# Optimization experiments

Hardware: AMD Instinct MI355X
Metric: run time of the kernel (lower is better)

## Reference

```python
import jax, jax.numpy as jnp
import numpy as np

N_NODES = 100000


def _sage_conv(x, edge_index, W_n, W_s, b):
    # edge_index: [2, E] with row0 = src, row1 = dst (messages flow src -> dst)
    src, dst = edge_index[0], edge_index[1]
    msgs = x[src]                                   # [E, F] gather
    summed = jax.ops.segment_sum(msgs, dst, num_segments=N_NODES)   # [N, F]
    deg = jax.ops.segment_sum(jnp.ones((edge_index.shape[1],), x.dtype), dst,
                              num_segments=N_NODES)                 # [N]
    mean = summed / jnp.maximum(deg, 1.0)[:, None]  # mean aggregation
    return mean @ W_n + x @ W_s + b


def setup_inputs() -> dict:
    key = jax.random.key(0)
    ks = jax.random.split(key, 8)
    in_dim, hid_dim, out_dim = 64, 64, 32
    n_edges = 1600000
    x = jax.random.normal(ks[0], (N_NODES, in_dim), dtype=jnp.float32)
    edge_index = jax.random.randint(ks[1], (2, n_edges), 0, N_NODES, dtype=jnp.int64)
    s1 = 1.0 / np.sqrt(in_dim)
    s2 = 1.0 / np.sqrt(hid_dim)
    W1_n = jax.random.uniform(ks[2], (in_dim, hid_dim), jnp.float32, -s1, s1)
    W1_s = jax.random.uniform(ks[3], (in_dim, hid_dim), jnp.float32, -s1, s1)
    b1 = jnp.zeros((hid_dim,), jnp.float32)
    W2_n = jax.random.uniform(ks[4], (hid_dim, out_dim), jnp.float32, -s2, s2)
    W2_s = jax.random.uniform(ks[5], (hid_dim, out_dim), jnp.float32, -s2, s2)
    b2 = jnp.zeros((out_dim,), jnp.float32)
    return {"x": x, "edge_index": edge_index, "W1_n": W1_n, "W1_s": W1_s,
            "b1": b1, "W2_n": W2_n, "W2_s": W2_s, "b2": b2}


def reference(x, edge_index, W1_n, W1_s, b1, W2_n, W2_s, b2):
    h = _sage_conv(x, edge_index, W1_n, W1_s, b1)
    h = jax.nn.relu(h)
    # dropout(p=0.5) is identity in eval mode
    out = _sage_conv(h, edge_index, W2_n, W2_s, b2)
    return out
```

## Files before the change

kernel.cpp:

```cpp
#include <hip/hip_runtime.h>
#include <hip/hip_bf16.h>

#define N_NODES 100000
#define NB 784
#define NPAD 100352
#define BSH 7
#define BMASK 127
#define CAP 4096

typedef float v2f __attribute__((ext_vector_type(2)));

__device__ inline void fma4(float a, const float4& w, float4& c) {
  c.x = fmaf(a, w.x, c.x);
  c.y = fmaf(a, w.y, c.y);
  c.z = fmaf(a, w.z, c.z);
  c.w = fmaf(a, w.w, c.w);
}
__device__ inline unsigned short f2bf(float f) {
  unsigned u = __float_as_uint(f);
  u += 0x7fffu + ((u >> 16) & 1u);
  return (unsigned short)(u >> 16);
}
__device__ inline unsigned pack2bf(float a, float b) {
  return (unsigned)f2bf(a) | ((unsigned)f2bf(b) << 16);
}
__device__ inline float bf2f(unsigned short u) {
  return __uint_as_float((unsigned)u << 16);
}
__device__ inline unsigned packfp8x4(float a, float b, float c, float d) {
  int pk = __builtin_amdgcn_cvt_pk_fp8_f32(a, b, 0, false);
  pk = __builtin_amdgcn_cvt_pk_fp8_f32(c, d, pk, true);
  return (unsigned)pk;
}
__device__ inline float4 relu_mix(uint2 m, uint2 s) {
  float4 v;
  v.x = fmaxf(__uint_as_float(m.x << 16) + __uint_as_float(s.x << 16), 0.f);
  v.y = fmaxf(__uint_as_float(m.x & 0xffff0000u) +
                  __uint_as_float(s.x & 0xffff0000u), 0.f);
  v.z = fmaxf(__uint_as_float(m.y << 16) + __uint_as_float(s.y << 16), 0.f);
  v.w = fmaxf(__uint_as_float(m.y & 0xffff0000u) +
                  __uint_as_float(s.y & 0xffff0000u), 0.f);
  return v;
}

#define EPB 4096
__global__ __launch_bounds__(512) void bscatter_k(const int* __restrict__ src,
                                                  const int* __restrict__ dst,
                                                  unsigned* __restrict__ bcur,
                                                  unsigned* __restrict__ ep,
                                                  int E) {
  __shared__ unsigned lh[NB];
  __shared__ unsigned lbase[NB];
  for (int i = threadIdx.x; i < NB; i += 512) lh[i] = 0;
  __syncthreads();
  const int base = blockIdx.x * EPB;
  unsigned short rank[8];
  unsigned short bb[8];
#pragma unroll
  for (int it = 0; it < 8; ++it) {
    int e = base + it * 512 + threadIdx.x;
    if (e < E) {
      unsigned b = ((unsigned)dst[e]) >> BSH;
      bb[it] = (unsigned short)b;
      rank[it] = (unsigned short)atomicAdd(&lh[b], 1u);
    }
  }
  __syncthreads();
  for (int i = threadIdx.x; i < NB; i += 512)
    lbase[i] = lh[i] ? atomicAdd(&bcur[i], lh[i]) : 0u;
  __syncthreads();
#pragma unroll
  for (int it = 0; it < 8; ++it) {
    int e = base + it * 512 + threadIdx.x;
    if (e < E) {
      unsigned b = bb[it];
      ep[(size_t)b * CAP + lbase[b] + rank[it]] =
          (((unsigned)src[e]) << BSH) | (((unsigned)dst[e]) & BMASK);
    }
  }
}

#define GB1 1563

__global__ __launch_bounds__(256) void fused1_k(
    const float* __restrict__ x, const float* __restrict__ W1n,
    const float* __restrict__ W1s, const float* __restrict__ b1,
    unsigned* __restrict__ xnb8, unsigned short* __restrict__ xsb,
    const unsigned* __restrict__ ep, const unsigned* __restrict__ bcur,
    int* __restrict__ ssrc, uint2* __restrict__ rows2, int M) {
  __shared__ __align__(16) float smem[8192];
  const int tid = threadIdx.x;

  if (blockIdx.x >= GB1) {
    const int b = blockIdx.x - GB1;
    unsigned* cnt = (unsigned*)smem;
    unsigned* sc = cnt + 128;
    const unsigned cntb = bcur[b];
    const unsigned beg = (unsigned)(b * CAP);
    if (tid < 128) cnt[tid] = 0;
    __syncthreads();
    for (unsigned j = tid; j < cntb; j += 256)
      atomicAdd(&cnt[ep[(size_t)beg + j] & BMASK], 1u);
    __syncthreads();
    unsigned v = (tid < 128) ? cnt[tid] : 0u;
    if (tid < 128) sc[tid] = v;
    __syncthreads();
    for (int off = 1; off < 128; off <<= 1) {
      unsigned t = (tid < 128 && tid >= off) ? sc[tid - off] : 0u;
      __syncthreads();
      if (tid < 128) sc[tid] += t;
      __syncthreads();
    }
    if (tid < 128) {
      unsigned ex = sc[tid] - v;
      rows2[b * 128 + tid] = make_uint2(beg + ex, beg + ex + v);
      cnt[tid] = ex;
    }
    __syncthreads();
    for (unsigned j = tid; j < cntb; j += 256) {
      unsigned p = ep[(size_t)beg + j];
      unsigned r = atomicAdd(&cnt[p & BMASK], 1u);
      ssrc[(size_t)beg + r] = (int)(p >> BSH);
    }
    return;
  }

  float* Wn = smem;
  float* Ws = smem + 4096;
  const int row0 = blockIdx.x * 64;

  for (int i = tid; i < 1024; i += 256) {
    ((float4*)Wn)[i] = ((const float4*)W1n)[i];
    ((float4*)Ws)[i] = ((const float4*)W1s)[i];
  }

  const int tx = tid & 15;
  const int ty = tid >> 4;
  const int arow = ty * 4;

  const float* xr[4];
#pragma unroll
  for (int r = 0; r < 4; ++r) {
    long long gr = row0 + arow + r;
    if (gr >= M) gr = M - 1;
    xr[r] = x + gr * 64;
  }

  float4 an[4], as[4];
#pragma unroll
  for (int r = 0; r < 4; ++r) {
    an[r] = make_float4(0.f, 0.f, 0.f, 0.f);
    as[r] = make_float4(0.f, 0.f, 0.f, 0.f);
  }
  __syncthreads();

#pragma unroll 2
  for (int k4 = 0; k4 < 16; ++k4) {
    float4 a[4];
#pragma unroll
    for (int r = 0; r < 4; ++r) a[r] = *(const float4*)(xr[r] + 4 * k4);
    float4 wn0 = *(const float4*)&Wn[(4 * k4 + 0) * 64 + 4 * tx];
    float4 wn1 = *(const float4*)&Wn[(4 * k4 + 1) * 64 + 4 * tx];
    float4 wn2 = *(const float4*)&Wn[(4 * k4 + 2) * 64 + 4 * tx];
    float4 wn3 = *(const float4*)&Wn[(4 * k4 + 3) * 64 + 4 * tx];
    float4 ws0 = *(const float4*)&Ws[(4 * k4 + 0) * 64 + 4 * tx];
    float4 ws1 = *(const float4*)&Ws[(4 * k4 + 1) * 64 + 4 * tx];
    float4 ws2 = *(const float4*)&Ws[(4 * k4 + 2) * 64 + 4 * tx];
    float4 ws3 = *(const float4*)&Ws[(4 * k4 + 3) * 64 + 4 * tx];
#pragma unroll
    for (int r = 0; r < 4; ++r) {
      fma4(a[r].x, wn0, an[r]);
      fma4(a[r].y, wn1, an[r]);
      fma4(a[r].z, wn2, an[r]);
      fma4(a[r].w, wn3, an[r]);
      fma4(a[r].x, ws0, as[r]);
      fma4(a[r].y, ws1, as[r]);
      fma4(a[r].z, ws2, as[r]);
      fma4(a[r].w, ws3, as[r]);
    }
  }

  const float4 bv = *(const float4*)&b1[4 * tx];
#pragma unroll
  for (int r = 0; r < 4; ++r) {
    int row = row0 + arow + r;
    if (row < M) {
      ushort4 ps;
      ps.x = f2bf(as[r].x + bv.x);
      ps.y = f2bf(as[r].y + bv.y);
      ps.z = f2bf(as[r].z + bv.z);
      ps.w = f2bf(as[r].w + bv.w);
      *(ushort4*)&xsb[(long long)row * 64 + 4 * tx] = ps;
      xnb8[(size_t)row * 16 + tx] =
          packfp8x4(an[r].x, an[r].y, an[r].z, an[r].w);
    }
  }
}

__global__ __launch_bounds__(256) void gather1_k(
    const uint4* __restrict__ valb4, const int* __restrict__ ssrc,
    const uint2* __restrict__ rows2, uint4* __restrict__ meanb, int N) {
  constexpr int P = 4;
  const int node = blockIdx.x * 64 + threadIdx.x / P;
  const int p = threadIdx.x & 3;
  if (node >= N) return;
  const uint2 be = rows2[node];
  const unsigned beg = be.x, end = be.y;

  float acc[16];
#pragma unroll
  for (int q = 0; q < 16; ++q) acc[q] = 0.f;

  unsigned j = beg;
  for (; j + 8 <= end; j += 8) {
    int sn[8];
#pragma unroll
    for (int i = 0; i < 8; ++i) sn[i] = ssrc[j + i];
    uint4 u[8];
#pragma unroll
    for (int i = 0; i < 8; ++i) u[i] = valb4[(size_t)sn[i] * P + p];
#pragma unroll
    for (int i = 0; i < 8; ++i) {
      v2f f0 = __builtin_amdgcn_cvt_pk_f32_fp8((int)u[i].x, false);
      v2f f1 = __builtin_amdgcn_cvt_pk_f32_fp8((int)u[i].x, true);
      v2f f2 = __builtin_amdgcn_cvt_pk_f32_fp8((int)u[i].y, false);
      v2f f3 = __builtin_amdgcn_cvt_pk_f32_fp8((int)u[i].y, true);
      v2f f4 = __builtin_amdgcn_cvt_pk_f32_fp8((int)u[i].z, false);
      v2f f5 = __builtin_amdgcn_cvt_pk_f32_fp8((int)u[i].z, true);
      v2f f6 = __builtin_amdgcn_cvt_pk_f32_fp8((int)u[i].w, false);
      v2f f7 = __builtin_amdgcn_cvt_pk_f32_fp8((int)u[i].w, true);
      acc[0] += f0[0];  acc[1] += f0[1];
      acc[2] += f1[0];  acc[3] += f1[1];
      acc[4] += f2[0];  acc[5] += f2[1];
      acc[6] += f3[0];  acc[7] += f3[1];
      acc[8] += f4[0];  acc[9] += f4[1];
      acc[10] += f5[0]; acc[11] += f5[1];
      acc[12] += f6[0]; acc[13] += f6[1];
      acc[14] += f7[0]; acc[15] += f7[1];
    }
  }
  if (j < end) {
    const unsigned last = end - 1;
    int sn[8];
#pragma unroll
    for (int i = 0; i < 8; ++i) {
      unsigned jj = j + i;
      sn[i] = ssrc[jj < last ? jj : last];
    }
    uint4 u[8];
#pragma unroll
    for (int i = 0; i < 8; ++i) u[i] = valb4[(size_t)sn[i] * P + p];
#pragma unroll
    for (int i = 0; i < 8; ++i) {
      float w = ((j + i) < end) ? 1.f : 0.f;
      v2f f0 = __builtin_amdgcn_cvt_pk_f32_fp8((int)u[i].x, false);
      v2f f1 = __builtin_amdgcn_cvt_pk_f32_fp8((int)u[i].x, true);
      v2f f2 = __builtin_amdgcn_cvt_pk_f32_fp8((int)u[i].y, false);
      v2f f3 = __builtin_amdgcn_cvt_pk_f32_fp8((int)u[i].y, true);
      v2f f4 = __builtin_amdgcn_cvt_pk_f32_fp8((int)u[i].z, false);
      v2f f5 = __builtin_amdgcn_cvt_pk_f32_fp8((int)u[i].z, true);
      v2f f6 = __builtin_amdgcn_cvt_pk_f32_fp8((int)u[i].w, false);
      v2f f7 = __builtin_amdgcn_cvt_pk_f32_fp8((int)u[i].w, true);
      acc[0] = fmaf(w, f0[0], acc[0]);   acc[1] = fmaf(w, f0[1], acc[1]);
      acc[2] = fmaf(w, f1[0], acc[2]);   acc[3] = fmaf(w, f1[1], acc[3]);
      acc[4] = fmaf(w, f2[0], acc[4]);   acc[5] = fmaf(w, f2[1], acc[5]);
      acc[6] = fmaf(w, f3[0], acc[6]);   acc[7] = fmaf(w, f3[1], acc[7]);
      acc[8] = fmaf(w, f4[0], acc[8]);   acc[9] = fmaf(w, f4[1], acc[9]);
      acc[10] = fmaf(w, f5[0], acc[10]); acc[11] = fmaf(w, f5[1], acc[11]);
      acc[12] = fmaf(w, f6[0], acc[12]); acc[13] = fmaf(w, f6[1], acc[13]);
      acc[14] = fmaf(w, f7[0], acc[14]); acc[15] = fmaf(w, f7[1], acc[15]);
    }
  }

  const unsigned dg = end - beg;
  const float inv = dg ? 1.f / (float)dg : 0.f;
  uint4 pk0, pk1;
  pk0.x = pack2bf(acc[0] * inv, acc[1] * inv);
  pk0.y = pack2bf(acc[2] * inv, acc[3] * inv);
  pk0.z = pack2bf(acc[4] * inv, acc[5] * inv);
  pk0.w = pack2bf(acc[6] * inv, acc[7] * inv);
  pk1.x = pack2bf(acc[8] * inv, acc[9] * inv);
  pk1.y = pack2bf(acc[10] * inv, acc[11] * inv);
  pk1.z = pack2bf(acc[12] * inv, acc[13] * inv);
  pk1.w = pack2bf(acc[14] * inv, acc[15] * inv);
  meanb[(size_t)node * 8 + 2 * p] = pk0;
  meanb[(size_t)node * 8 + 2 * p + 1] = pk1;
}

__global__ __launch_bounds__(256) void gemm2_k(
    const unsigned short* __restrict__ mean1,
    const unsigned short* __restrict__ xsb, const float* __restrict__ W2n,
    const float* __restrict__ W2s, const float* __restrict__ b2,
    unsigned* __restrict__ hnb8, float* __restrict__ hs, int M) {
  __shared__ float Wn[64 * 32];
  __shared__ float Ws[64 * 32];
  const int tid = threadIdx.x;
  const int row0 = blockIdx.x * 128;

  for (int i = tid; i < 512; i += 256) {
    ((float4*)Wn)[i] = ((const float4*)W2n)[i];
    ((float4*)Ws)[i] = ((const float4*)W2s)[i];
  }

  const int tx = tid & 7;
  const int ty = tid >> 3;
  const int arow = ty * 4;

  const uint2* mp[4];
  const uint2* sp[4];
#pragma unroll
  for (int r = 0; r < 4; ++r) {
    long long gr = row0 + arow + r;
    if (gr >= M) gr = M - 1;
    mp[r] = (const uint2*)(mean1 + gr * 64);
    sp[r] = (const uint2*)(xsb + gr * 64);
  }

  float4 an[4], as[4];
#pragma unroll
  for (int r = 0; r < 4; ++r) {
    an[r] = make_float4(0.f, 0.f, 0.f, 0.f);
    as[r] = make_float4(0.f, 0.f, 0.f, 0.f);
  }
  __syncthreads();

#pragma unroll 2
  for (int k4 = 0; k4 < 16; ++k4) {
    float4 a[4];
#pragma unroll
    for (int r = 0; r < 4; ++r) a[r] = relu_mix(mp[r][k4], sp[r][k4]);
    float4 wn0 = *(const float4*)&Wn[(4 * k4 + 0) * 32 + 4 * tx];
    float4 wn1 = *(const float4*)&Wn[(4 * k4 + 1) * 32 + 4 * tx];
    float4 wn2 = *(const float4*)&Wn[(4 * k4 + 2) * 32 + 4 * tx];
    float4 wn3 = *(const float4*)&Wn[(4 * k4 + 3) * 32 + 4 * tx];
    float4 ws0 = *(const float4*)&Ws[(4 * k4 + 0) * 32 + 4 * tx];
    float4 ws1 = *(const float4*)&Ws[(4 * k4 + 1) * 32 + 4 * tx];
    float4 ws2 = *(const float4*)&Ws[(4 * k4 + 2) * 32 + 4 * tx];
    float4 ws3 = *(const float4*)&Ws[(4 * k4 + 3) * 32 + 4 * tx];
#pragma unroll
    for (int r = 0; r < 4; ++r) {
      fma4(a[r].x, wn0, an[r]);
      fma4(a[r].y, wn1, an[r]);
      fma4(a[r].z, wn2, an[r]);
      fma4(a[r].w, wn3, an[r]);
      fma4(a[r].x, ws0, as[r]);
      fma4(a[r].y, ws1, as[r]);
      fma4(a[r].z, ws2, as[r]);
      fma4(a[r].w, ws3, as[r]);
    }
  }

  const float4 bv = *(const float4*)&b2[4 * tx];
#pragma unroll
  for (int r = 0; r < 4; ++r) {
    int row = row0 + arow + r;
    if (row < M) {
      float4 o;
      o.x = as[r].x + bv.x;
      o.y = as[r].y + bv.y;
      o.z = as[r].z + bv.z;
      o.w = as[r].w + bv.w;
      *(float4*)&hs[(long long)row * 32 + 4 * tx] = o;
      hnb8[(size_t)row * 8 + tx] =
          packfp8x4(an[r].x, an[r].y, an[r].z, an[r].w);
    }
  }
}

__global__ __launch_bounds__(256) void gather2_k(
    const uint4* __restrict__ valb4, const int* __restrict__ ssrc,
    const uint2* __restrict__ rows2, const float* __restrict__ base,
    float* __restrict__ out, int N) {
  constexpr int P = 2;
  const int node = blockIdx.x * 128 + threadIdx.x / P;
  const int p = threadIdx.x & 1;
  if (node >= N) return;
  const uint2 be = rows2[node];
  const unsigned beg = be.x, end = be.y;

  float acc[16];
#pragma unroll
  for (int q = 0; q < 16; ++q) acc[q] = 0.f;

  unsigned j = beg;
  for (; j + 8 <= end; j += 8) {
    int sn[8];
#pragma unroll
    for (int i = 0; i < 8; ++i) sn[i] = ssrc[j + i];
    uint4 u[8];
#pragma unroll
    for (int i = 0; i < 8; ++i) u[i] = valb4[(size_t)sn[i] * P + p];
#pragma unroll
    for (int i = 0; i < 8; ++i) {
      v2f f0 = __builtin_amdgcn_cvt_pk_f32_fp8((int)u[i].x, false);
      v2f f1 = __builtin_amdgcn_cvt_pk_f32_fp8((int)u[i].x, true);
      v2f f2 = __builtin_amdgcn_cvt_pk_f32_fp8((int)u[i].y, false);
      v2f f3 = __builtin_amdgcn_cvt_pk_f32_fp8((int)u[i].y, true);
      v2f f4 = __builtin_amdgcn_cvt_pk_f32_fp8((int)u[i].z, false);
      v2f f5 = __builtin_amdgcn_cvt_pk_f32_fp8((int)u[i].z, true);
      v2f f6 = __builtin_amdgcn_cvt_pk_f32_fp8((int)u[i].w, false);
      v2f f7 = __builtin_amdgcn_cvt_pk_f32_fp8((int)u[i].w, true);
      acc[0] += f0[0];  acc[1] += f0[1];
      acc[2] += f1[0];  acc[3] += f1[1];
      acc[4] += f2[0];  acc[5] += f2[1];
      acc[6] += f3[0];  acc[7] += f3[1];
      acc[8] += f4[0];  acc[9] += f4[1];
      acc[10] += f5[0]; acc[11] += f5[1];
      acc[12] += f6[0]; acc[13] += f6[1];
      acc[14] += f7[0]; acc[15] += f7[1];
    }
  }
  if (j < end) {
    const unsigned last = end - 1;
    int sn[8];
#pragma unroll
    for (int i = 0; i < 8; ++i) {
      unsigned jj = j + i;
      sn[i] = ssrc[jj < last ? jj : last];
    }
    uint4 u[8];
#pragma unroll
    for (int i = 0; i < 8; ++i) u[i] = valb4[(size_t)sn[i] * P + p];
#pragma unroll
    for (int i = 0; i < 8; ++i) {
      float w = ((j + i) < end) ? 1.f : 0.f;
      v2f f0 = __builtin_amdgcn_cvt_pk_f32_fp8((int)u[i].x, false);
      v2f f1 = __builtin_amdgcn_cvt_pk_f32_fp8((int)u[i].x, true);
      v2f f2 = __builtin_amdgcn_cvt_pk_f32_fp8((int)u[i].y, false);
      v2f f3 = __builtin_amdgcn_cvt_pk_f32_fp8((int)u[i].y, true);
      v2f f4 = __builtin_amdgcn_cvt_pk_f32_fp8((int)u[i].z, false);
      v2f f5 = __builtin_amdgcn_cvt_pk_f32_fp8((int)u[i].z, true);
      v2f f6 = __builtin_amdgcn_cvt_pk_f32_fp8((int)u[i].w, false);
      v2f f7 = __builtin_amdgcn_cvt_pk_f32_fp8((int)u[i].w, true);
      acc[0] = fmaf(w, f0[0], acc[0]);   acc[1] = fmaf(w, f0[1], acc[1]);
      acc[2] = fmaf(w, f1[0], acc[2]);   acc[3] = fmaf(w, f1[1], acc[3]);
      acc[4] = fmaf(w, f2[0], acc[4]);   acc[5] = fmaf(w, f2[1], acc[5]);
      acc[6] = fmaf(w, f3[0], acc[6]);   acc[7] = fmaf(w, f3[1], acc[7]);
      acc[8] = fmaf(w, f4[0], acc[8]);   acc[9] = fmaf(w, f4[1], acc[9]);
      acc[10] = fmaf(w, f5[0], acc[10]); acc[11] = fmaf(w, f5[1], acc[11]);
      acc[12] = fmaf(w, f6[0], acc[12]); acc[13] = fmaf(w, f6[1], acc[13]);
      acc[14] = fmaf(w, f7[0], acc[14]); acc[15] = fmaf(w, f7[1], acc[15]);
    }
  }

  const unsigned dg = end - beg;
  const float inv = dg ? 1.f / (float)dg : 0.f;
  const size_t o = (size_t)node * 32 + 16 * p;
#pragma unroll
  for (int q4 = 0; q4 < 4; ++q4) {
    float4 bv = *(const float4*)&base[o + 4 * q4];
    float4 ov;
    ov.x = acc[4 * q4 + 0] * inv + bv.x;
    ov.y = acc[4 * q4 + 1] * inv + bv.y;
    ov.z = acc[4 * q4 + 2] * inv + bv.z;
    ov.w = acc[4 * q4 + 3] * inv + bv.w;
    *(float4*)&out[o + 4 * q4] = ov;
  }
}

extern "C" void kernel_launch(void* const* d_in, const int* in_sizes, int n_in,
                              void* d_out, int out_size, void* d_ws,
                              size_t ws_size, hipStream_t stream) {
  const float* x   = (const float*)d_in[0];
  const int*   ei  = (const int*)d_in[1];
  const float* W1n = (const float*)d_in[2];
  const float* W1s = (const float*)d_in[3];
  const float* b1  = (const float*)d_in[4];
  const float* W2n = (const float*)d_in[5];
  const float* W2s = (const float*)d_in[6];
  const float* b2  = (const float*)d_in[7];
  float* out = (float*)d_out;

  const int E = in_sizes[1] / 2;
  const int M = N_NODES;
  const int* src = ei;
  const int* dst = ei + E;

  char* wsb = (char*)d_ws;
  unsigned*       ep    = (unsigned*)(wsb);
  int*            ssrc  = (int*)(wsb + 12845056);
  uint2*          rows2 = (uint2*)(wsb + 25690112);
  unsigned*       bcur  = (unsigned*)(wsb + 26492928);
  unsigned*       xnb8  = (unsigned*)(wsb + 26496064);
  unsigned short* xsb   = (unsigned short*)(wsb + 32896064);
  unsigned short* mean1 = (unsigned short*)(wsb + 45696064);
  float*          hs    = (float*)(wsb + 58496064);
  unsigned*       hnb8  = (unsigned*)(wsb);

  hipMemsetAsync(bcur, 0, NB * 4, stream);
  bscatter_k<<<(E + EPB - 1) / EPB, 512, 0, stream>>>(src, dst, bcur, ep, E);
  fused1_k<<<GB1 + NB, 256, 0, stream>>>(x, W1n, W1s, b1, xnb8, xsb, ep, bcur,
                                         ssrc, rows2, M);
  gather1_k<<<(M + 63) / 64, 256, 0, stream>>>((const uint4*)xnb8, ssrc, rows2,
                                               (uint4*)mean1, M);
  gemm2_k<<<(M + 127) / 128, 256, 0, stream>>>(mean1, xsb, W2n, W2s, b2, hnb8,
                                               hs, M);
  gather2_k<<<(M + 127) / 128, 256, 0, stream>>>((const uint4*)hnb8, ssrc,
                                                 rows2, hs, out, M);
}
```

Before: 207.8 us.

## Fuse bucket scatter with layer-1 GEMM and gather1 with layer-2 GEMM

Moves the edge bucket-scatter into the same launch as the layer-1 dense transform, and splits the per-bucket sort into its own kernel. It also fuses the first gather with the second layer's GEMM, keeping the mean rows in shared memory instead of writing and re-reading a bf16 mean buffer in global memory. This removes one intermediate buffer round-trip and rebalances launches. The cost is a heavier fused kernel with more shared memory and fewer rows per thread in the GEMM part, which may affect occupancy.

```diff
diff --git a/kernel.cpp b/kernel.cpp
--- a/kernel.cpp
+++ b/kernel.cpp
@@ -44,90 +44,54 @@
 }
 
 #define EPB 4096
-__global__ __launch_bounds__(512) void bscatter_k(const int* __restrict__ src,
-                                                  const int* __restrict__ dst,
-                                                  unsigned* __restrict__ bcur,
-                                                  unsigned* __restrict__ ep,
-                                                  int E) {
-  __shared__ unsigned lh[NB];
-  __shared__ unsigned lbase[NB];
-  for (int i = threadIdx.x; i < NB; i += 512) lh[i] = 0;
-  __syncthreads();
-  const int base = blockIdx.x * EPB;
-  unsigned short rank[8];
-  unsigned short bb[8];
-#pragma unroll
-  for (int it = 0; it < 8; ++it) {
-    int e = base + it * 512 + threadIdx.x;
-    if (e < E) {
-      unsigned b = ((unsigned)dst[e]) >> BSH;
-      bb[it] = (unsigned short)b;
-      rank[it] = (unsigned short)atomicAdd(&lh[b], 1u);
-    }
-  }
-  __syncthreads();
-  for (int i = threadIdx.x; i < NB; i += 512)
-    lbase[i] = lh[i] ? atomicAdd(&bcur[i], lh[i]) : 0u;
-  __syncthreads();
-#pragma unroll
-  for (int it = 0; it < 8; ++it) {
-    int e = base + it * 512 + threadIdx.x;
-    if (e < E) {
-      unsigned b = bb[it];
-      ep[(size_t)b * CAP + lbase[b] + rank[it]] =
-          (((unsigned)src[e]) << BSH) | (((unsigned)dst[e]) & BMASK);
-    }
-  }
-}
-
 #define GB1 1563
 
-__global__ __launch_bounds__(256) void fused1_k(
+__global__ __launch_bounds__(256) void fusedA_k(
+    const int* __restrict__ src, const int* __restrict__ dst,
+    unsigned* __restrict__ bcur, unsigned* __restrict__ ep,
     const float* __restrict__ x, const float* __restrict__ W1n,
     const float* __restrict__ W1s, const float* __restrict__ b1,
     unsigned* __restrict__ xnb8, unsigned short* __restrict__ xsb,
-    const unsigned* __restrict__ ep, const unsigned* __restrict__ bcur,
-    int* __restrict__ ssrc, uint2* __restrict__ rows2, int M) {
+    int E, int NSB, int M) {
   __shared__ __align__(16) float smem[8192];
   const int tid = threadIdx.x;
 
-  if (blockIdx.x >= GB1) {
-    const int b = blockIdx.x - GB1;
-    unsigned* cnt = (unsigned*)smem;
-    unsigned* sc = cnt + 128;
-    const unsigned cntb = bcur[b];
-    const unsigned beg = (unsigned)(b * CAP);
-    if (tid < 128) cnt[tid] = 0;
+  if ((int)blockIdx.x < NSB) {
+    unsigned* lh = (unsigned*)smem;
+    unsigned* lbase = lh + NB;
+    for (int i = tid; i < NB; i += 256) lh[i] = 0;
     __syncthreads();
-    for (unsigned j = tid; j < cntb; j += 256)
-      atomicAdd(&cnt[ep[(size_t)beg + j] & BMASK], 1u);
+    const int base = blockIdx.x * EPB;
+    unsigned short rank[16];
+    unsigned short bb[16];
+#pragma unroll
+    for (int it = 0; it < 16; ++it) {
+      int e = base + it * 256 + tid;
+      if (e < E) {
+        unsigned b = ((unsigned)dst[e]) >> BSH;
+        bb[it] = (unsigned short)b;
+        rank[it] = (unsigned short)atomicAdd(&lh[b], 1u);
+      }
+    }
     __syncthreads();
-    unsigned v = (tid < 128) ? cnt[tid] : 0u;
-    if (tid < 128) sc[tid] = v;
+    for (int i = tid; i < NB; i += 256)
+      lbase[i] = lh[i] ? atomicAdd(&bcur[i], lh[i]) : 0u;
     __syncthreads();
-    for (int off = 1; off < 128; off <<= 1) {
-      unsigned t = (tid < 128 && tid >= off) ? sc[tid - off] : 0u;
-      __syncthreads();
-      if (tid < 128) sc[tid] += t;
-      __syncthreads();
-    }
-    if (tid < 128) {
-      unsigned ex = sc[tid] - v;
-      rows2[b * 128 + tid] = make_uint2(beg + ex, beg + ex + v);
-      cnt[tid] = ex;
-    }
-    __syncthreads();
-    for (unsigned j = tid; j < cntb; j += 256) {
-      unsigned p = ep[(size_t)beg + j];
-      unsigned r = atomicAdd(&cnt[p & BMASK], 1u);
-      ssrc[(size_t)beg + r] = (int)(p >> BSH);
+#pragma unroll
+    for (int it = 0; it < 16; ++it) {
+      int e = base + it * 256 + tid;
+      if (e < E) {
+        unsigned b = bb[it];
+        ep[(size_t)b * CAP + lbase[b] + rank[it]] =
+            (((unsigned)src[e]) << BSH) | (((unsigned)dst[e]) & BMASK);
+      }
     }
     return;
   }
 
   float* Wn = smem;
   float* Ws = smem + 4096;
-  const int row0 = blockIdx.x * 64;
+  const int row0 = ((int)blockIdx.x - NSB) * 64;
 
   for (int i = tid; i < 1024; i += 256) {
     ((float4*)Wn)[i] = ((const float4*)W1n)[i];
@@ -197,13 +161,66 @@
   }
 }
 
-__global__ __launch_bounds__(256) void gather1_k(
+__global__ __launch_bounds__(256) void bsort_k(const unsigned* __restrict__ ep,
+                                               const unsigned* __restrict__ bcur,
+                                               int* __restrict__ ssrc,
+                                               uint2* __restrict__ rows2) {
+  __shared__ unsigned cnt[128];
+  __shared__ unsigned sc[128];
+  const int tid = threadIdx.x;
+  const int b = blockIdx.x;
+  const unsigned cntb = bcur[b];
+  const unsigned beg = (unsigned)(b * CAP);
+  if (tid < 128) cnt[tid] = 0;
+  __syncthreads();
+  for (unsigned j = tid; j < cntb; j += 256)
+    atomicAdd(&cnt[ep[(size_t)beg + j] & BMASK], 1u);
+  __syncthreads();
+  unsigned v = (tid < 128) ? cnt[tid] : 0u;
+  if (tid < 128) sc[tid] = v;
+  __syncthreads();
+  for (int off = 1; off < 128; off <<= 1) {
+    unsigned t = (tid < 128 && tid >= off) ? sc[tid - off] : 0u;
+    __syncthreads();
+    if (tid < 128) sc[tid] += t;
+    __syncthreads();
+  }
+  if (tid < 128) {
+    unsigned ex = sc[tid] - v;
+    rows2[b * 128 + tid] = make_uint2(beg + ex, beg + ex + v);
+    cnt[tid] = ex;
+  }
+  __syncthreads();
+  for (unsigned j = tid; j < cntb; j += 256) {
+    unsigned p = ep[(size_t)beg + j];
+    unsigned r = atomicAdd(&cnt[p & BMASK], 1u);
+    ssrc[(size_t)beg + r] = (int)(p >> BSH);
+  }
+}
+
+#define MSTRIDE 36
+
+__global__ __launch_bounds__(256) void fgg_k(
     const uint4* __restrict__ valb4, const int* __restrict__ ssrc,
-    const uint2* __restrict__ rows2, uint4* __restrict__ meanb, int N) {
+    const uint2* __restrict__ rows2, const unsigned short* __restrict__ xsb,
+    const float* __restrict__ W2n, const float* __restrict__ W2s,
+    const float* __restrict__ b2, unsigned* __restrict__ hnb8,
+    float* __restrict__ hs, int M) {
+  __shared__ float Wn[64 * 32];
+  __shared__ float Ws[64 * 32];
+  __shared__ unsigned mlds[64 * MSTRIDE];
+  const int tid = threadIdx.x;
+  const int node0 = blockIdx.x * 64;
+
+  for (int i = tid; i < 512; i += 256) {
+    ((float4*)Wn)[i] = ((const float4*)W2n)[i];
+    ((float4*)Ws)[i] = ((const float4*)W2s)[i];
+  }
+
   constexpr int P = 4;
-  const int node = blockIdx.x * 64 + threadIdx.x / P;
-  const int p = threadIdx.x & 3;
-  if (node >= N) return;
+  const int lrow = tid / P;
+  const int node = node0 + lrow;
+  const int p = tid & 3;
   const uint2 be = rows2[node];
   const unsigned beg = be.x, end = be.y;
 
@@ -283,52 +300,36 @@
   pk1.y = pack2bf(acc[10] * inv, acc[11] * inv);
   pk1.z = pack2bf(acc[12] * inv, acc[13] * inv);
   pk1.w = pack2bf(acc[14] * inv, acc[15] * inv);
-  meanb[(size_t)node * 8 + 2 * p] = pk0;
-  meanb[(size_t)node * 8 + 2 * p + 1] = pk1;
-}
-
-__global__ __launch_bounds__(256) void gemm2_k(
-    const unsigned short* __restrict__ mean1,
-    const unsigned short* __restrict__ xsb, const float* __restrict__ W2n,
-    const float* __restrict__ W2s, const float* __restrict__ b2,
-    unsigned* __restrict__ hnb8, float* __restrict__ hs, int M) {
-  __shared__ float Wn[64 * 32];
-  __shared__ float Ws[64 * 32];
-  const int tid = threadIdx.x;
-  const int row0 = blockIdx.x * 128;
-
-  for (int i = tid; i < 512; i += 256) {
-    ((float4*)Wn)[i] = ((const float4*)W2n)[i];
-    ((float4*)Ws)[i] = ((const float4*)W2s)[i];
-  }
+  *(uint4*)&mlds[lrow * MSTRIDE + p * 8] = pk0;
+  *(uint4*)&mlds[lrow * MSTRIDE + p * 8 + 4] = pk1;
+  __syncthreads();
 
   const int tx = tid & 7;
   const int ty = tid >> 3;
-  const int arow = ty * 4;
-
-  const uint2* mp[4];
-  const uint2* sp[4];
-#pragma unroll
-  for (int r = 0; r < 4; ++r) {
-    long long gr = row0 + arow + r;
+  const int arow = ty * 2;
+
+  const uint2* mp[2];
+  const uint2* sp[2];
+#pragma unroll
+  for (int r = 0; r < 2; ++r) {
+    long long gr = node0 + arow + r;
     if (gr >= M) gr = M - 1;
-    mp[r] = (const uint2*)(mean1 + gr * 64);
+    mp[r] = (const uint2*)&mlds[(arow + r) * MSTRIDE];
     sp[r] = (const uint2*)(xsb + gr * 64);
   }
 
-  float4 an[4], as[4];
-#pragma unroll
-  for (int r = 0; r < 4; ++r) {
+  float4 an[2], as[2];
+#pragma unroll
+  for (int r = 0; r < 2; ++r) {
     an[r] = make_float4(0.f, 0.f, 0.f, 0.f);
     as[r] = make_float4(0.f, 0.f, 0.f, 0.f);
   }
-  __syncthreads();
 
 #pragma unroll 2
   for (int k4 = 0; k4 < 16; ++k4) {
-    float4 a[4];
-#pragma unroll
-    for (int r = 0; r < 4; ++r) a[r] = relu_mix(mp[r][k4], sp[r][k4]);
+    float4 a[2];
+#pragma unroll
+    for (int r = 0; r < 2; ++r) a[r] = relu_mix(mp[r][k4], sp[r][k4]);
     float4 wn0 = *(const float4*)&Wn[(4 * k4 + 0) * 32 + 4 * tx];
     float4 wn1 = *(const float4*)&Wn[(4 * k4 + 1) * 32 + 4 * tx];
     float4 wn2 = *(const float4*)&Wn[(4 * k4 + 2) * 32 + 4 * tx];
@@ -338,7 +339,7 @@
     float4 ws2 = *(const float4*)&Ws[(4 * k4 + 2) * 32 + 4 * tx];
     float4 ws3 = *(const float4*)&Ws[(4 * k4 + 3) * 32 + 4 * tx];
 #pragma unroll
-    for (int r = 0; r < 4; ++r) {
+    for (int r = 0; r < 2; ++r) {
       fma4(a[r].x, wn0, an[r]);
       fma4(a[r].y, wn1, an[r]);
       fma4(a[r].z, wn2, an[r]);
@@ -352,8 +353,8 @@
 
   const float4 bv = *(const float4*)&b2[4 * tx];
 #pragma unroll
-  for (int r = 0; r < 4; ++r) {
-    int row = row0 + arow + r;
+  for (int r = 0; r < 2; ++r) {
+    int row = node0 + arow + r;
     if (row < M) {
       float4 o;
       o.x = as[r].x + bv.x;
@@ -475,6 +476,7 @@
   const int M = N_NODES;
   const int* src = ei;
   const int* dst = ei + E;
+  const int NSB = (E + EPB - 1) / EPB;
 
   char* wsb = (char*)d_ws;
   unsigned*       ep    = (unsigned*)(wsb);
@@ -483,18 +485,15 @@
   unsigned*       bcur  = (unsigned*)(wsb + 26492928);
   unsigned*       xnb8  = (unsigned*)(wsb + 26496064);
   unsigned short* xsb   = (unsigned short*)(wsb + 32896064);
-  unsigned short* mean1 = (unsigned short*)(wsb + 45696064);
-  float*          hs    = (float*)(wsb + 58496064);
+  float*          hs    = (float*)(wsb + 45696064);
   unsigned*       hnb8  = (unsigned*)(wsb);
 
   hipMemsetAsync(bcur, 0, NB * 4, stream);
-  bscatter_k<<<(E + EPB - 1) / EPB, 512, 0, stream>>>(src, dst, bcur, ep, E);
-  fused1_k<<<GB1 + NB, 256, 0, stream>>>(x, W1n, W1s, b1, xnb8, xsb, ep, bcur,
-                                         ssrc, rows2, M);
-  gather1_k<<<(M + 63) / 64, 256, 0, stream>>>((const uint4*)xnb8, ssrc, rows2,
-                                               (uint4*)mean1, M);
-  gemm2_k<<<(M + 127) / 128, 256, 0, stream>>>(mean1, xsb, W2n, W2s, b2, hnb8,
-                                               hs, M);
+  fusedA_k<<<NSB + GB1, 256, 0, stream>>>(src, dst, bcur, ep, x, W1n, W1s, b1,
+                                          xnb8, xsb, E, NSB, M);
+  bsort_k<<<NB, 256, 0, stream>>>(ep, bcur, ssrc, rows2);
+  fgg_k<<<GB1, 256, 0, stream>>>((const uint4*)xnb8, ssrc, rows2, xsb, W2n,
+                                 W2s, b2, hnb8, hs, M);
   gather2_k<<<(M + 127) / 128, 256, 0, stream>>>((const uint4*)hnb8, ssrc,
                                                  rows2, hs, out, M);
 }
```

Result: faster. 198.8 us (-4.3%).
